# Performance work log

Hardware: AMD Instinct MI355X
Metric: run time of the kernel (lower is better)

Reference implementation:

```python
import jax, jax.numpy as jnp
import numpy as np

N, DIM, T = 4096, 100, 50
DT = np.float32(1.0 / T)          # delta_t = total_time / num_time_interval
R = 1.0                           # fbsde._R
Q = 1.0                           # state cost in h_th
DELTA_CLIP = 50.0
UMIN, UMAX = -1.0, 1.0            # config.u_threhold_min/max
EPS = 1e-6                        # BatchNorm eps


def _bn(x, w, b):
    # BatchNorm1d in training mode: batch stats, biased variance
    m = jnp.mean(x, axis=0)
    v = jnp.mean((x - m) ** 2, axis=0)
    return (x - m) * jax.lax.rsqrt(v + EPS) * w + b


def _subnet(x, p):
    # FCSubNet: bn -> [linear(no bias) -> bn -> relu] x2 -> linear(bias) -> bn -> /dim
    (bn0_w, bn0_b, w1, bn1_w, bn1_b, w2, bn2_w, bn2_b, w3, b3, bn3_w, bn3_b) = p
    h = _bn(x, bn0_w, bn0_b)
    h = jax.nn.relu(_bn(h @ w1.T, bn1_w, bn1_b))
    h = jax.nn.relu(_bn(h @ w2.T, bn2_w, bn2_b))
    h = h @ w3.T + b3
    return _bn(h, bn3_w, bn3_b) / DIM


def setup_inputs() -> dict:
    key = jax.random.key(0)
    ks = jax.random.split(key, 15)
    s = 0.05  # keep weights small for numerical stability over 50 recurrent steps
    return dict(
        dw=jax.random.normal(ks[0], (N, DIM, T), jnp.float32) * jnp.sqrt(DT),
        y_init=jax.random.uniform(ks[1], (1,), jnp.float32, 0.0, 1.0),
        z_init=jax.random.uniform(ks[2], (1, DIM), jnp.float32, -0.1, 0.1),
        bn0_w=jax.random.uniform(ks[3], (100,), jnp.float32, 0.1, 0.5),
        bn0_b=jax.random.normal(ks[4], (100,), jnp.float32) * 0.1,
        w1=jax.random.normal(ks[5], (110, 100), jnp.float32) * s,
        bn1_w=jax.random.uniform(ks[6], (110,), jnp.float32, 0.1, 0.5),
        bn1_b=jax.random.normal(ks[7], (110,), jnp.float32) * 0.1,
        w2=jax.random.normal(ks[8], (110, 110), jnp.float32) * s,
        bn2_w=jax.random.uniform(ks[9], (110,), jnp.float32, 0.1, 0.5),
        bn2_b=jax.random.normal(ks[10], (110,), jnp.float32) * 0.1,
        w3=jax.random.normal(ks[11], (100, 110), jnp.float32) * s,
        b3=jax.random.normal(ks[12], (100,), jnp.float32) * s,
        bn3_w=jax.random.uniform(ks[13], (100,), jnp.float32, 0.1, 0.5),
        bn3_b=jax.random.normal(ks[14], (100,), jnp.float32) * 0.1,
    )


def reference(dw, y_init, z_init, bn0_w, bn0_b, w1, bn1_w, bn1_b, w2, bn2_w, bn2_b,
              w3, b3, bn3_w, bn3_b):
    p = (bn0_w, bn0_b, w1, bn1_w, bn1_b, w2, bn2_w, bn2_b, w3, b3, bn3_w, bn3_b)
    n = dw.shape[0]
    gamma = jnp.ones((n, DIM, 1), dw.dtype)          # fbsde.gamma; sigma@gamma = gamma (sigma=I), G = ones
    y = jnp.broadcast_to(y_init, (n, 1))[:, :, None]  # [n,1,1]
    z = jnp.broadcast_to(z_init, (n, DIM))[:, :, None]  # [n,dim,1]
    x = jnp.zeros((n, DIM, 1), dw.dtype)
    dw_t = jnp.moveaxis(dw, 2, 0)[..., None]          # [T, n, dim, 1]

    def y_update(x, y, z, u, dwi):
        h = 0.5 * (Q * jnp.sum(x * x, axis=1, keepdims=True) + R * u * u)  # h_th -> [n,1,1]
        i2 = DT * jnp.sum(z * gamma, axis=1, keepdims=True) * u
        i3 = jnp.sum(z * dwi, axis=1, keepdims=True)
        return y - DT * h + i2 + i3

    def step(carry, dwi):
        x, y, z = carry
        u = jnp.clip(-(1.0 / R) * jnp.sum(gamma * z, axis=1, keepdims=True), UMIN, UMAX)
        y = y_update(x, y, z, u, dwi)
        # x_{t+1} = x + f(x)*dt + sigma@gamma*u*dt + G*dw ; f(x) = -x
        x_new = x - x * DT + gamma * u * DT + dwi
        z_new = (_subnet(x_new[:, :, 0], p) / DIM)[:, :, None]
        return (x_new, y, z_new), (x[:, :, 0], u[:, 0, 0])

    (x, y, z), (xs, us) = jax.lax.scan(step, (x, y, z), dw_t[:-1])
    # final step t = T-1: only u and y are updated (loop breaks before x/z update)
    u = jnp.clip(-(1.0 / R) * jnp.sum(gamma * z, axis=1, keepdims=True), UMIN, UMAX)
    y = y_update(x, y, z, u, dw_t[-1])
    xs = jnp.concatenate([xs, x[None, :, :, 0]], axis=0)   # [T, n, dim] = totalx
    us = jnp.concatenate([us, u[None, :, 0, 0]], axis=0)   # [T, n]     = totalu

    ye = 0.5 * jnp.sum(x[:, :, 0] ** 2, axis=1, keepdims=True)  # g_th -> [n,1]
    d = y[:, :, 0] - ye
    ad = jnp.abs(d)
    sl1 = jnp.mean(jnp.where(ad < 1.0, 0.5 * d * d, ad - 0.5))  # SmoothL1Loss, beta=1
    loss = 2.0 * DELTA_CLIP * (sl1 + jnp.mean(ye[:, 0]) ** 2)
    return loss, y, ye, xs, us
```

## Files before the change

kernel.cpp:

```cpp
#include <hip/hip_runtime.h>

#define NS    4096
#define DDIM  100
#define HD    110
#define HP    112
#define TSTEPS 50
#define DTc   0.02f
#define EPSc  1e-6f

__global__ void kw_prep(const float* __restrict__ w1, const float* __restrict__ w2,
                        const float* __restrict__ w3,
                        float* __restrict__ wtt1, float* __restrict__ wtt2,
                        float* __restrict__ wtt3) {
  int tid = threadIdx.x;
  for (int idx = tid; idx < 14 * 100 * 8; idx += 256) {
    int jt = idx / 800, r = idx % 800, k = r / 8, jj = r % 8, j = jt * 8 + jj;
    wtt1[idx] = (j < HD) ? w1[j * DDIM + k] : 0.f;
  }
  for (int idx = tid; idx < 14 * 110 * 8; idx += 256) {
    int jt = idx / 880, r = idx % 880, k = r / 8, jj = r % 8, j = jt * 8 + jj;
    wtt2[idx] = (j < HD) ? w2[j * HD + k] : 0.f;
  }
  for (int idx = tid; idx < 13 * 110 * 8; idx += 256) {
    int jt = idx / 880, r = idx % 880, k = r / 8, jj = r % 8, j = jt * 8 + jj;
    wtt3[idx] = (j < DDIM) ? w3[j * HD + k] : 0.f;
  }
}

__global__ __launch_bounds__(256) void kt_dw(const float* __restrict__ dw,
                                             float* __restrict__ dwT) {
  int n = blockIdx.x * 256 + threadIdx.x;
  int d = blockIdx.y;
  const float2* src = (const float2*)(dw + (size_t)n * DDIM * TSTEPS + d * TSTEPS);
  float v[TSTEPS];
#pragma unroll
  for (int i = 0; i < TSTEPS / 2; ++i) {
    float2 p = src[i];
    v[2 * i] = p.x; v[2 * i + 1] = p.y;
  }
#pragma unroll
  for (int t = 0; t < TSTEPS; ++t)
    dwT[((size_t)t * DDIM + d) * NS + n] = v[t];
}

__global__ __launch_bounds__(1024) void ka2(
    int t, int flags,
    const float* __restrict__ dw, const float* __restrict__ dwT,
    const float* __restrict__ y_init, const float* __restrict__ z_init,
    const float* __restrict__ bn3w, const float* __restrict__ bn3b,
    float* __restrict__ x, float* __restrict__ y, const float* __restrict__ h3,
    const float* __restrict__ stats3, float* __restrict__ stats0,
    float* __restrict__ st_zero, float* __restrict__ lacc,
    float* __restrict__ out_y, float* __restrict__ out_ye,
    float* __restrict__ out_xs, float* __restrict__ out_us)
{
  const bool first  = flags & 1;
  const bool last_  = flags & 2;
  const bool usedwt = flags & 4;
  int tid = threadIdx.x, lane = tid & 63, w = tid >> 6;
  int n = blockIdx.x * 64 + lane;
  int d0 = w * 7;
  int nd = DDIM - d0; nd = nd < 0 ? 0 : (nd > 7 ? 7 : nd);

  __shared__ float2 zp[DDIM];
  __shared__ float ps[3][16][64];
  __shared__ float ush[64];
  __shared__ float pst[2][112];

  if (blockIdx.x == 0 && tid < 224) st_zero[tid] = 0.f;
  if (!first && tid < DDIM) {
    float m = stats3[tid] * (1.f / NS);
    float v = stats3[HP + tid] * (1.f / NS) - m * m;
    float istd = rsqrtf(v + EPSc);
    float A = istd * bn3w[tid] * 1e-4f;
    float B = (bn3b[tid] - m * istd * bn3w[tid]) * 1e-4f;
    zp[tid] = make_float2(A, B);
  }
  __syncthreads();

  float xv[7], dwv[7];
  float pz = 0.f, pzdw = 0.f, px2 = 0.f;
#pragma unroll
  for (int i = 0; i < 7; ++i) {
    if (i < nd) {
      int d = d0 + i;
      float zd = first ? z_init[d] : fmaf(h3[d * NS + n], zp[d].x, zp[d].y);
      dwv[i] = usedwt ? dwT[((size_t)t * DDIM + d) * NS + n]
                      : dw[(size_t)n * DDIM * TSTEPS + d * TSTEPS + t];
      xv[i] = first ? 0.f : x[d * NS + n];
      pz += zd;
      pzdw = fmaf(zd, dwv[i], pzdw);
      px2 = fmaf(xv[i], xv[i], px2);
    }
  }
  ps[0][w][lane] = pz; ps[1][w][lane] = pzdw; ps[2][w][lane] = px2;
  __syncthreads();

  if (w == 0) {
    float sz = 0.f, szdw = 0.f, sx2 = 0.f;
#pragma unroll
    for (int k = 0; k < 16; ++k) {
      sz += ps[0][k][lane]; szdw += ps[1][k][lane]; sx2 += ps[2][k][lane];
    }
    float u = fminf(fmaxf(-sz, -1.f), 1.f);
    float yv = first ? y_init[0] : y[n];
    yv += -DTc * 0.5f * (sx2 + u * u) + DTc * sz * u + szdw;
    out_us[t * NS + n] = u;
    ush[lane] = u;
    if (!last_) {
      y[n] = yv;
    } else {
      out_y[n] = yv;
      float ye = 0.5f * sx2;
      out_ye[n] = ye;
      float dd = yv - ye, ad = fabsf(dd);
      float s = ad < 1.f ? 0.5f * dd * dd : ad - 0.5f;
      float q = ye;
      for (int off = 32; off; off >>= 1) {
        s += __shfl_down(s, off);
        q += __shfl_down(q, off);
      }
      if (lane == 0) { atomicAdd(&lacc[0], s); atomicAdd(&lacc[1], q); }
    }
  }
  __syncthreads();

  if (!last_) {
    float u = ush[lane];
#pragma unroll
    for (int i = 0; i < 7; ++i) {
      if (i < nd) {
        int d = d0 + i;
        float xn = fmaf(xv[i], 1.f - DTc, fmaf(u, DTc, dwv[i]));
        x[d * NS + n] = xn;
        out_xs[((size_t)t * NS + n) * DDIM + d] = xv[i];
        float s = xn, q = xn * xn;
        for (int off = 32; off; off >>= 1) {
          s += __shfl_down(s, off);
          q += __shfl_down(q, off);
        }
        if (lane == 0) { pst[0][d] = s; pst[1][d] = q; }
      }
    }
    __syncthreads();
    if (tid < DDIM) atomicAdd(&stats0[tid], pst[0][tid]);
    else if (tid >= 128 && tid < 128 + DDIM) atomicAdd(&stats0[HP + tid - 128], pst[1][tid - 128]);
  } else {
#pragma unroll
    for (int i = 0; i < 7; ++i)
      if (i < nd)
        out_xs[((size_t)t * NS + n) * DDIM + i + d0] = xv[i];
  }
}

template <int KD, int RELU, int HASB>
__global__ __launch_bounds__(64) void km2(
    const float* __restrict__ in, float* __restrict__ out,
    const float* __restrict__ stats_in, float* __restrict__ stats_out,
    float* __restrict__ zero_ptr,
    const float* __restrict__ bnw, const float* __restrict__ bnb,
    const float* __restrict__ wtt, const float* __restrict__ bias, int Jreal)
{
  int tid = threadIdx.x;
  int jt = blockIdx.y;
  int n = blockIdx.x * 64 + tid;

  __shared__ float4 wl[KD * 2];
  __shared__ float2 ab[KD];

  const float4* src = (const float4*)(wtt + (size_t)jt * KD * 8);
  for (int i = tid; i < KD * 2; i += 64) wl[i] = src[i];
  for (int k = tid; k < KD; k += 64) {
    float m = stats_in[k] * (1.f / NS);
    float v = stats_in[HP + k] * (1.f / NS) - m * m;
    float istd = rsqrtf(v + EPSc);
    float A = istd * bnw[k];
    ab[k] = make_float2(A, bnb[k] - m * A);
  }
  if (blockIdx.x == 0 && jt == 0)
    for (int i = tid; i < 224; i += 64) zero_ptr[i] = 0.f;
  __syncthreads();

  float acc[8] = {0, 0, 0, 0, 0, 0, 0, 0};
  const float* ip = in + n;
#pragma unroll 10
  for (int k = 0; k < KD; ++k) {
    float a = ip[(size_t)k * NS];
    float2 p = ab[k];
    a = fmaf(a, p.x, p.y);
    if (RELU) a = fmaxf(a, 0.f);
    float4 wA = wl[2 * k], wB = wl[2 * k + 1];
    acc[0] = fmaf(a, wA.x, acc[0]); acc[1] = fmaf(a, wA.y, acc[1]);
    acc[2] = fmaf(a, wA.z, acc[2]); acc[3] = fmaf(a, wA.w, acc[3]);
    acc[4] = fmaf(a, wB.x, acc[4]); acc[5] = fmaf(a, wB.y, acc[5]);
    acc[6] = fmaf(a, wB.z, acc[6]); acc[7] = fmaf(a, wB.w, acc[7]);
  }

  int j0 = jt * 8;
#pragma unroll
  for (int jj = 0; jj < 8; ++jj) {
    int j = j0 + jj;
    if (j < Jreal) {
      float vv = acc[jj] + (HASB ? bias[j] : 0.f);
      out[j * NS + n] = vv;
      float s = vv, q = vv * vv;
      for (int off = 32; off; off >>= 1) {
        s += __shfl_down(s, off);
        q += __shfl_down(q, off);
      }
      if (tid == 0) {
        atomicAdd(&stats_out[j], s);
        atomicAdd(&stats_out[HP + j], q);
      }
    }
  }
}

__global__ void k_loss(const float* __restrict__ lacc, float* __restrict__ out_loss) {
  float sl1 = lacc[0] * (1.f / NS);
  float mye = lacc[1] * (1.f / NS);
  out_loss[0] = 100.f * (sl1 + mye * mye);
}

extern "C" void kernel_launch(void* const* d_in, const int* in_sizes, int n_in,
                              void* d_out, int out_size, void* d_ws, size_t ws_size,
                              hipStream_t stream) {
  const float* dw     = (const float*)d_in[0];
  const float* y_init = (const float*)d_in[1];
  const float* z_init = (const float*)d_in[2];
  const float* bn0w   = (const float*)d_in[3];
  const float* bn0b   = (const float*)d_in[4];
  const float* w1     = (const float*)d_in[5];
  const float* bn1w   = (const float*)d_in[6];
  const float* bn1b   = (const float*)d_in[7];
  const float* w2     = (const float*)d_in[8];
  const float* bn2w   = (const float*)d_in[9];
  const float* bn2b   = (const float*)d_in[10];
  const float* w3     = (const float*)d_in[11];
  const float* b3     = (const float*)d_in[12];
  const float* bn3w   = (const float*)d_in[13];
  const float* bn3b   = (const float*)d_in[14];

  float* ws  = (float*)d_ws;
  float* x   = ws;
  float* y   = x + 409600;
  float* h1  = y + 4096;
  float* h2  = h1 + (size_t)HP * NS;
  float* h3  = h2 + (size_t)HP * NS;
  float* st  = h3 + (size_t)HP * NS;
  float* st0 = st, *st1 = st + 224, *st2 = st + 448, *st3 = st + 672;
  float* lacc = st + 896;
  float* wtt1 = lacc + 8;
  float* wtt2 = wtt1 + 14 * 100 * 8;
  float* wtt3 = wtt2 + 14 * 110 * 8;
  float* dwT  = wtt3 + 13 * 110 * 8;
  size_t need_dwt = ((size_t)(dwT - ws) + (size_t)TSTEPS * DDIM * NS) * sizeof(float);
  bool usedwt = ws_size >= need_dwt;

  float* out      = (float*)d_out;
  float* out_loss = out;
  float* out_y    = out + 1;
  float* out_ye   = out_y + NS;
  float* out_xs   = out_ye + NS;
  float* out_us   = out_xs + (size_t)TSTEPS * NS * DDIM;

  hipMemsetAsync(st, 0, (896 + 8) * sizeof(float), stream);
  kw_prep<<<1, 256, 0, stream>>>(w1, w2, w3, wtt1, wtt2, wtt3);
  if (usedwt) kt_dw<<<dim3(16, 100), 256, 0, stream>>>(dw, dwT);

  for (int t = 0; t < TSTEPS; ++t) {
    int flags = (t == 0 ? 1 : 0) | (t == TSTEPS - 1 ? 2 : 0) | (usedwt ? 4 : 0);
    ka2<<<64, 1024, 0, stream>>>(t, flags, dw, dwT, y_init, z_init,
                                 bn3w, bn3b, x, y, h3, st3, st0, st2, lacc,
                                 out_y, out_ye, out_xs, out_us);
    if (t < TSTEPS - 1) {
      km2<100, 0, 0><<<dim3(64, 14), 64, 0, stream>>>(
          x, h1, st0, st1, st3, bn0w, bn0b, wtt1, (const float*)nullptr, HD);
      km2<110, 1, 0><<<dim3(64, 14), 64, 0, stream>>>(
          h1, h2, st1, st2, st0, bn1w, bn1b, wtt2, (const float*)nullptr, HD);
      km2<110, 1, 1><<<dim3(64, 13), 64, 0, stream>>>(
          h2, h3, st2, st3, st1, bn2w, bn2b, wtt3, b3, DDIM);
    }
  }
  k_loss<<<1, 1, 0, stream>>>(lacc, out_loss);
}
```

Before: 5.628 ms.

## Fuse all timesteps into one cooperative persistent kernel with grid barriers

```diff
diff --git a/kernel.cpp b/kernel.cpp
--- a/kernel.cpp
+++ b/kernel.cpp
@@ -1,113 +1,125 @@
 #include <hip/hip_runtime.h>
 
-#define NS    4096
-#define DDIM  100
-#define HD    110
-#define HP    112
+#define NS     4096
+#define DDIM   100
+#define HD     110
+#define JP     128
+#define HP     112
 #define TSTEPS 50
-#define DTc   0.02f
-#define EPSc  1e-6f
-
-__global__ void kw_prep(const float* __restrict__ w1, const float* __restrict__ w2,
-                        const float* __restrict__ w3,
-                        float* __restrict__ wtt1, float* __restrict__ wtt2,
-                        float* __restrict__ wtt3) {
-  int tid = threadIdx.x;
-  for (int idx = tid; idx < 14 * 100 * 8; idx += 256) {
-    int jt = idx / 800, r = idx % 800, k = r / 8, jj = r % 8, j = jt * 8 + jj;
-    wtt1[idx] = (j < HD) ? w1[j * DDIM + k] : 0.f;
-  }
-  for (int idx = tid; idx < 14 * 110 * 8; idx += 256) {
-    int jt = idx / 880, r = idx % 880, k = r / 8, jj = r % 8, j = jt * 8 + jj;
-    wtt2[idx] = (j < HD) ? w2[j * HD + k] : 0.f;
-  }
-  for (int idx = tid; idx < 13 * 110 * 8; idx += 256) {
-    int jt = idx / 880, r = idx % 880, k = r / 8, jj = r % 8, j = jt * 8 + jj;
-    wtt3[idx] = (j < DDIM) ? w3[j * HD + k] : 0.f;
-  }
-}
-
-__global__ __launch_bounds__(256) void kt_dw(const float* __restrict__ dw,
-                                             float* __restrict__ dwT) {
-  int n = blockIdx.x * 256 + threadIdx.x;
-  int d = blockIdx.y;
-  const float2* src = (const float2*)(dw + (size_t)n * DDIM * TSTEPS + d * TSTEPS);
-  float v[TSTEPS];
-#pragma unroll
-  for (int i = 0; i < TSTEPS / 2; ++i) {
-    float2 p = src[i];
-    v[2 * i] = p.x; v[2 * i + 1] = p.y;
-  }
-#pragma unroll
-  for (int t = 0; t < TSTEPS; ++t)
-    dwT[((size_t)t * DDIM + d) * NS + n] = v[t];
-}
-
-__global__ __launch_bounds__(1024) void ka2(
-    int t, int flags,
-    const float* __restrict__ dw, const float* __restrict__ dwT,
-    const float* __restrict__ y_init, const float* __restrict__ z_init,
-    const float* __restrict__ bn3w, const float* __restrict__ bn3b,
-    float* __restrict__ x, float* __restrict__ y, const float* __restrict__ h3,
-    const float* __restrict__ stats3, float* __restrict__ stats0,
-    float* __restrict__ st_zero, float* __restrict__ lacc,
-    float* __restrict__ out_y, float* __restrict__ out_ye,
-    float* __restrict__ out_xs, float* __restrict__ out_us)
-{
-  const bool first  = flags & 1;
-  const bool last_  = flags & 2;
-  const bool usedwt = flags & 4;
+#define DTc    0.02f
+#define EPSc   1e-6f
+#define NB     256
+#define BT     512
+
+struct MegaArgs {
+  const float *dw, *y_init, *z_init;
+  const float *bn0w, *bn0b, *w1, *bn1w, *bn1b, *w2, *bn2w, *bn2b, *w3, *b3, *bn3w, *bn3b;
+  float *x, *y, *h1, *h2, *h3;
+  float *st0, *st1, *st2, *st3, *lacc;
+  float *wt1, *wt2, *wt3, *dwT;
+  int *cnt; int usedwt;
+  float *out_loss, *out_y, *out_ye, *out_xs, *out_us;
+};
+
+__device__ __forceinline__ void gbar(int* cnt, int idx) {
+  __syncthreads();
+  if (threadIdx.x == 0) {
+    __threadfence();
+    atomicAdd(&cnt[idx], 1);
+    while (__hip_atomic_load(&cnt[idx], __ATOMIC_RELAXED, __HIP_MEMORY_SCOPE_AGENT) < NB)
+      __builtin_amdgcn_s_sleep(1);
+    __threadfence();
+  }
+  __syncthreads();
+}
+
+__device__ void init_phase(const float* __restrict__ w1, const float* __restrict__ w2,
+                           const float* __restrict__ w3,
+                           float* __restrict__ wt1, float* __restrict__ wt2,
+                           float* __restrict__ wt3,
+                           const float* __restrict__ dw, float* __restrict__ dwT,
+                           int usedwt) {
+  int g = blockIdx.x * BT + threadIdx.x;
+  for (int idx = g; idx < DDIM * JP; idx += NB * BT) {
+    int k = idx >> 7, j = idx & 127;
+    wt1[idx] = (j < HD) ? w1[j * DDIM + k] : 0.f;
+  }
+  for (int idx = g; idx < HD * JP; idx += NB * BT) {
+    int k = idx >> 7, j = idx & 127;
+    wt2[idx] = (j < HD) ? w2[j * HD + k] : 0.f;
+    wt3[idx] = (j < DDIM) ? w3[j * HD + k] : 0.f;
+  }
+  if (usedwt) {
+    int n = g & (NS - 1);
+    int d0 = g >> 12;
+    for (int d = d0; d < DDIM; d += 32) {
+      const float2* src = (const float2*)(dw + (size_t)n * DDIM * TSTEPS + d * TSTEPS);
+      float v[TSTEPS];
+#pragma unroll
+      for (int i = 0; i < TSTEPS / 2; ++i) { float2 p = src[i]; v[2*i] = p.x; v[2*i+1] = p.y; }
+#pragma unroll
+      for (int tt = 0; tt < TSTEPS; ++tt)
+        dwT[((size_t)tt * DDIM + d) * NS + n] = v[tt];
+    }
+  }
+}
+
+template <int LAST>
+__device__ void p0_phase(int t, int first, int usedwt,
+                         const float* __restrict__ dwT, const float* __restrict__ dwraw,
+                         const float* __restrict__ y_init, const float* __restrict__ z_init,
+                         const float* __restrict__ bn3w, const float* __restrict__ bn3b,
+                         float* __restrict__ x, float* __restrict__ y,
+                         const float* __restrict__ h3, const float* __restrict__ st3,
+                         float* __restrict__ st0, float* __restrict__ lacc,
+                         float* __restrict__ out_y, float* __restrict__ out_ye,
+                         float* __restrict__ out_xs, float* __restrict__ out_us,
+                         float2* zp, float* ps, float* ush, float* zero_target) {
   int tid = threadIdx.x, lane = tid & 63, w = tid >> 6;
-  int n = blockIdx.x * 64 + lane;
-  int d0 = w * 7;
-  int nd = DDIM - d0; nd = nd < 0 ? 0 : (nd > 7 ? 7 : nd);
-
-  __shared__ float2 zp[DDIM];
-  __shared__ float ps[3][16][64];
-  __shared__ float ush[64];
-  __shared__ float pst[2][112];
-
-  if (blockIdx.x == 0 && tid < 224) st_zero[tid] = 0.f;
+  int bid = blockIdx.x;
+  if (bid >= 64) {
+    if (bid == 64 && tid < 2 * HP) zero_target[tid] = 0.f;
+    return;
+  }
+  int n = bid * 64 + lane;
   if (!first && tid < DDIM) {
-    float m = stats3[tid] * (1.f / NS);
-    float v = stats3[HP + tid] * (1.f / NS) - m * m;
+    float m = st3[tid] * (1.f / NS);
+    float v = st3[HP + tid] * (1.f / NS) - m * m;
     float istd = rsqrtf(v + EPSc);
     float A = istd * bn3w[tid] * 1e-4f;
     float B = (bn3b[tid] - m * istd * bn3w[tid]) * 1e-4f;
     zp[tid] = make_float2(A, B);
   }
   __syncthreads();
-
-  float xv[7], dwv[7];
+  int d0 = w * 13;
+  int cd = DDIM - d0; cd = cd > 13 ? 13 : cd;
+  float xr[13], dwr[13];
   float pz = 0.f, pzdw = 0.f, px2 = 0.f;
 #pragma unroll
-  for (int i = 0; i < 7; ++i) {
-    if (i < nd) {
-      int d = d0 + i;
-      float zd = first ? z_init[d] : fmaf(h3[d * NS + n], zp[d].x, zp[d].y);
-      dwv[i] = usedwt ? dwT[((size_t)t * DDIM + d) * NS + n]
-                      : dw[(size_t)n * DDIM * TSTEPS + d * TSTEPS + t];
-      xv[i] = first ? 0.f : x[d * NS + n];
-      pz += zd;
-      pzdw = fmaf(zd, dwv[i], pzdw);
-      px2 = fmaf(xv[i], xv[i], px2);
-    }
-  }
-  ps[0][w][lane] = pz; ps[1][w][lane] = pzdw; ps[2][w][lane] = px2;
-  __syncthreads();
-
+  for (int i = 0; i < 13; ++i) if (i < cd) {
+    int d = d0 + i;
+    float zd = first ? z_init[d] : fmaf(h3[(size_t)d * NS + n], zp[d].x, zp[d].y);
+    dwr[i] = usedwt ? dwT[((size_t)t * DDIM + d) * NS + n]
+                    : dwraw[(size_t)n * DDIM * TSTEPS + d * TSTEPS + t];
+    xr[i] = first ? 0.f : x[(size_t)d * NS + n];
+    pz += zd; pzdw = fmaf(zd, dwr[i], pzdw); px2 = fmaf(xr[i], xr[i], px2);
+  }
+  ps[(0 * 8 + w) * 64 + lane] = pz;
+  ps[(1 * 8 + w) * 64 + lane] = pzdw;
+  ps[(2 * 8 + w) * 64 + lane] = px2;
+  __syncthreads();
   if (w == 0) {
     float sz = 0.f, szdw = 0.f, sx2 = 0.f;
 #pragma unroll
-    for (int k = 0; k < 16; ++k) {
-      sz += ps[0][k][lane]; szdw += ps[1][k][lane]; sx2 += ps[2][k][lane];
+    for (int k = 0; k < 8; ++k) {
+      sz += ps[k * 64 + lane]; szdw += ps[(8 + k) * 64 + lane]; sx2 += ps[(16 + k) * 64 + lane];
     }
     float u = fminf(fmaxf(-sz, -1.f), 1.f);
     float yv = first ? y_init[0] : y[n];
     yv += -DTc * 0.5f * (sx2 + u * u) + DTc * sz * u + szdw;
     out_us[t * NS + n] = u;
     ush[lane] = u;
-    if (!last_) {
+    if (!LAST) {
       y[n] = yv;
     } else {
       out_y[n] = yv;
@@ -116,171 +128,162 @@
       float dd = yv - ye, ad = fabsf(dd);
       float s = ad < 1.f ? 0.5f * dd * dd : ad - 0.5f;
       float q = ye;
-      for (int off = 32; off; off >>= 1) {
-        s += __shfl_down(s, off);
-        q += __shfl_down(q, off);
+      for (int off = 32; off; off >>= 1) { s += __shfl_down(s, off); q += __shfl_down(q, off); }
+      if (lane == 0) { atomicAdd(&lacc[0], s); atomicAdd(&lacc[1], q); }
+    }
+  }
+  __syncthreads();
+  if (!LAST) {
+    float u = ush[lane];
+#pragma unroll
+    for (int i = 0; i < 13; ++i) if (i < cd) {
+      int d = d0 + i;
+      float xn = fmaf(xr[i], 1.f - DTc, fmaf(u, DTc, dwr[i]));
+      x[(size_t)d * NS + n] = xn;
+      out_xs[((size_t)t * NS + n) * DDIM + d] = xr[i];
+      float s = xn, q = xn * xn;
+      for (int off = 32; off; off >>= 1) { s += __shfl_down(s, off); q += __shfl_down(q, off); }
+      if (lane == 0) { atomicAdd(&st0[d], s); atomicAdd(&st0[HP + d], q); }
+    }
+  } else {
+#pragma unroll
+    for (int i = 0; i < 13; ++i) if (i < cd)
+      out_xs[((size_t)(TSTEPS - 1) * NS + n) * DDIM + d0 + i] = xr[i];
+  }
+}
+
+template <int KD, int RELU, int HASB>
+__device__ void gemm_phase(const float* __restrict__ in, float* __restrict__ out,
+                           const float* __restrict__ stats_in, float* __restrict__ stats_out,
+                           const float* __restrict__ bnw, const float* __restrict__ bnb,
+                           const float* __restrict__ wt, const float* __restrict__ bias,
+                           int Jreal, float* ldsx, float2* ldsab, float* zero_target) {
+  int tid = threadIdx.x, lane = tid & 63, w = tid >> 6;
+  int n0 = (blockIdx.x & 63) * 64;
+  int jq = blockIdx.x >> 6;
+  if (tid < KD) {
+    float m = stats_in[tid] * (1.f / NS);
+    float v = stats_in[HP + tid] * (1.f / NS) - m * m;
+    float A = rsqrtf(v + EPSc) * bnw[tid];
+    ldsab[tid] = make_float2(A, bnb[tid] - m * A);
+  }
+  for (int k = w; k < KD; k += 8)
+    ldsx[k * 64 + lane] = in[(size_t)k * NS + n0 + lane];
+  if (blockIdx.x == 64 && w == 7) {
+    for (int i = lane; i < 2 * HP; i += 64) zero_target[i] = 0.f;
+  }
+  __syncthreads();
+  if (w < 7) {
+    int j0 = __builtin_amdgcn_readfirstlane(jq * 28 + w * 4);
+    const float* wp = wt + j0;
+    float a0 = 0.f, a1 = 0.f, a2 = 0.f, a3 = 0.f;
+#pragma unroll 5
+    for (int k = 0; k < KD; ++k) {
+      float a = ldsx[k * 64 + lane];
+      float2 p = ldsab[k];
+      a = fmaf(a, p.x, p.y);
+      if (RELU) a = fmaxf(a, 0.f);
+      const float* wr = wp + k * JP;
+      a0 = fmaf(a, wr[0], a0); a1 = fmaf(a, wr[1], a1);
+      a2 = fmaf(a, wr[2], a2); a3 = fmaf(a, wr[3], a3);
+    }
+    float acc[4] = {a0, a1, a2, a3};
+#pragma unroll
+    for (int i = 0; i < 4; ++i) {
+      int j = j0 + i;
+      if (j < Jreal) {
+        float vv = acc[i] + (HASB ? bias[j] : 0.f);
+        out[(size_t)j * NS + n0 + lane] = vv;
+        float s = vv, q = vv * vv;
+        for (int off = 32; off; off >>= 1) { s += __shfl_down(s, off); q += __shfl_down(q, off); }
+        if (lane == 0) { atomicAdd(&stats_out[j], s); atomicAdd(&stats_out[HP + j], q); }
       }
-      if (lane == 0) { atomicAdd(&lacc[0], s); atomicAdd(&lacc[1], q); }
-    }
-  }
-  __syncthreads();
-
-  if (!last_) {
-    float u = ush[lane];
-#pragma unroll
-    for (int i = 0; i < 7; ++i) {
-      if (i < nd) {
-        int d = d0 + i;
-        float xn = fmaf(xv[i], 1.f - DTc, fmaf(u, DTc, dwv[i]));
-        x[d * NS + n] = xn;
-        out_xs[((size_t)t * NS + n) * DDIM + d] = xv[i];
-        float s = xn, q = xn * xn;
-        for (int off = 32; off; off >>= 1) {
-          s += __shfl_down(s, off);
-          q += __shfl_down(q, off);
-        }
-        if (lane == 0) { pst[0][d] = s; pst[1][d] = q; }
-      }
-    }
-    __syncthreads();
-    if (tid < DDIM) atomicAdd(&stats0[tid], pst[0][tid]);
-    else if (tid >= 128 && tid < 128 + DDIM) atomicAdd(&stats0[HP + tid - 128], pst[1][tid - 128]);
-  } else {
-#pragma unroll
-    for (int i = 0; i < 7; ++i)
-      if (i < nd)
-        out_xs[((size_t)t * NS + n) * DDIM + i + d0] = xv[i];
-  }
-}
-
-template <int KD, int RELU, int HASB>
-__global__ __launch_bounds__(64) void km2(
-    const float* __restrict__ in, float* __restrict__ out,
-    const float* __restrict__ stats_in, float* __restrict__ stats_out,
-    float* __restrict__ zero_ptr,
-    const float* __restrict__ bnw, const float* __restrict__ bnb,
-    const float* __restrict__ wtt, const float* __restrict__ bias, int Jreal)
-{
-  int tid = threadIdx.x;
-  int jt = blockIdx.y;
-  int n = blockIdx.x * 64 + tid;
-
-  __shared__ float4 wl[KD * 2];
-  __shared__ float2 ab[KD];
-
-  const float4* src = (const float4*)(wtt + (size_t)jt * KD * 8);
-  for (int i = tid; i < KD * 2; i += 64) wl[i] = src[i];
-  for (int k = tid; k < KD; k += 64) {
-    float m = stats_in[k] * (1.f / NS);
-    float v = stats_in[HP + k] * (1.f / NS) - m * m;
-    float istd = rsqrtf(v + EPSc);
-    float A = istd * bnw[k];
-    ab[k] = make_float2(A, bnb[k] - m * A);
-  }
-  if (blockIdx.x == 0 && jt == 0)
-    for (int i = tid; i < 224; i += 64) zero_ptr[i] = 0.f;
-  __syncthreads();
-
-  float acc[8] = {0, 0, 0, 0, 0, 0, 0, 0};
-  const float* ip = in + n;
-#pragma unroll 10
-  for (int k = 0; k < KD; ++k) {
-    float a = ip[(size_t)k * NS];
-    float2 p = ab[k];
-    a = fmaf(a, p.x, p.y);
-    if (RELU) a = fmaxf(a, 0.f);
-    float4 wA = wl[2 * k], wB = wl[2 * k + 1];
-    acc[0] = fmaf(a, wA.x, acc[0]); acc[1] = fmaf(a, wA.y, acc[1]);
-    acc[2] = fmaf(a, wA.z, acc[2]); acc[3] = fmaf(a, wA.w, acc[3]);
-    acc[4] = fmaf(a, wB.x, acc[4]); acc[5] = fmaf(a, wB.y, acc[5]);
-    acc[6] = fmaf(a, wB.z, acc[6]); acc[7] = fmaf(a, wB.w, acc[7]);
-  }
-
-  int j0 = jt * 8;
-#pragma unroll
-  for (int jj = 0; jj < 8; ++jj) {
-    int j = j0 + jj;
-    if (j < Jreal) {
-      float vv = acc[jj] + (HASB ? bias[j] : 0.f);
-      out[j * NS + n] = vv;
-      float s = vv, q = vv * vv;
-      for (int off = 32; off; off >>= 1) {
-        s += __shfl_down(s, off);
-        q += __shfl_down(q, off);
-      }
-      if (tid == 0) {
-        atomicAdd(&stats_out[j], s);
-        atomicAdd(&stats_out[HP + j], q);
-      }
-    }
-  }
-}
-
-__global__ void k_loss(const float* __restrict__ lacc, float* __restrict__ out_loss) {
-  float sl1 = lacc[0] * (1.f / NS);
-  float mye = lacc[1] * (1.f / NS);
-  out_loss[0] = 100.f * (sl1 + mye * mye);
+    }
+  }
+}
+
+__global__ __launch_bounds__(BT, 1) void mega(MegaArgs a) {
+  __shared__ float  ldsx[HD * 64];
+  __shared__ float2 ldsab[HP];
+  __shared__ float2 zp[DDIM];
+  __shared__ float  ps[3 * 8 * 64];
+  __shared__ float  ush[64];
+
+  init_phase(a.w1, a.w2, a.w3, a.wt1, a.wt2, a.wt3, a.dw, a.dwT, a.usedwt);
+  int bi = 0;
+  gbar(a.cnt, bi++);
+
+  for (int t = 0; t < TSTEPS - 1; ++t) {
+    p0_phase<0>(t, t == 0, a.usedwt, a.dwT, a.dw, a.y_init, a.z_init, a.bn3w, a.bn3b,
+                a.x, a.y, a.h3, a.st3, a.st0, a.lacc, a.out_y, a.out_ye, a.out_xs, a.out_us,
+                zp, ps, ush, a.st2);
+    gbar(a.cnt, bi++);
+    gemm_phase<DDIM, 0, 0>(a.x,  a.h1, a.st0, a.st1, a.bn0w, a.bn0b, a.wt1, (const float*)0, HD,   ldsx, ldsab, a.st3);
+    gbar(a.cnt, bi++);
+    gemm_phase<HD,   1, 0>(a.h1, a.h2, a.st1, a.st2, a.bn1w, a.bn1b, a.wt2, (const float*)0, HD,   ldsx, ldsab, a.st0);
+    gbar(a.cnt, bi++);
+    gemm_phase<HD,   1, 1>(a.h2, a.h3, a.st2, a.st3, a.bn2w, a.bn2b, a.wt3, a.b3,            DDIM, ldsx, ldsab, a.st1);
+    gbar(a.cnt, bi++);
+  }
+  p0_phase<1>(TSTEPS - 1, 0, a.usedwt, a.dwT, a.dw, a.y_init, a.z_init, a.bn3w, a.bn3b,
+              a.x, a.y, a.h3, a.st3, a.st0, a.lacc, a.out_y, a.out_ye, a.out_xs, a.out_us,
+              zp, ps, ush, a.st2);
+  gbar(a.cnt, bi++);
+  if (blockIdx.x == 0 && threadIdx.x == 0) {
+    float sl1 = a.lacc[0] * (1.f / NS);
+    float mye = a.lacc[1] * (1.f / NS);
+    a.out_loss[0] = 100.f * (sl1 + mye * mye);
+  }
 }
 
 extern "C" void kernel_launch(void* const* d_in, const int* in_sizes, int n_in,
                               void* d_out, int out_size, void* d_ws, size_t ws_size,
                               hipStream_t stream) {
-  const float* dw     = (const float*)d_in[0];
-  const float* y_init = (const float*)d_in[1];
-  const float* z_init = (const float*)d_in[2];
-  const float* bn0w   = (const float*)d_in[3];
-  const float* bn0b   = (const float*)d_in[4];
-  const float* w1     = (const float*)d_in[5];
-  const float* bn1w   = (const float*)d_in[6];
-  const float* bn1b   = (const float*)d_in[7];
-  const float* w2     = (const float*)d_in[8];
-  const float* bn2w   = (const float*)d_in[9];
-  const float* bn2b   = (const float*)d_in[10];
-  const float* w3     = (const float*)d_in[11];
-  const float* b3     = (const float*)d_in[12];
-  const float* bn3w   = (const float*)d_in[13];
-  const float* bn3b   = (const float*)d_in[14];
-
-  float* ws  = (float*)d_ws;
-  float* x   = ws;
-  float* y   = x + 409600;
-  float* h1  = y + 4096;
-  float* h2  = h1 + (size_t)HP * NS;
-  float* h3  = h2 + (size_t)HP * NS;
-  float* st  = h3 + (size_t)HP * NS;
-  float* st0 = st, *st1 = st + 224, *st2 = st + 448, *st3 = st + 672;
-  float* lacc = st + 896;
-  float* wtt1 = lacc + 8;
-  float* wtt2 = wtt1 + 14 * 100 * 8;
-  float* wtt3 = wtt2 + 14 * 110 * 8;
-  float* dwT  = wtt3 + 13 * 110 * 8;
-  size_t need_dwt = ((size_t)(dwT - ws) + (size_t)TSTEPS * DDIM * NS) * sizeof(float);
-  bool usedwt = ws_size >= need_dwt;
-
-  float* out      = (float*)d_out;
-  float* out_loss = out;
-  float* out_y    = out + 1;
-  float* out_ye   = out_y + NS;
-  float* out_xs   = out_ye + NS;
-  float* out_us   = out_xs + (size_t)TSTEPS * NS * DDIM;
-
-  hipMemsetAsync(st, 0, (896 + 8) * sizeof(float), stream);
-  kw_prep<<<1, 256, 0, stream>>>(w1, w2, w3, wtt1, wtt2, wtt3);
-  if (usedwt) kt_dw<<<dim3(16, 100), 256, 0, stream>>>(dw, dwT);
-
-  for (int t = 0; t < TSTEPS; ++t) {
-    int flags = (t == 0 ? 1 : 0) | (t == TSTEPS - 1 ? 2 : 0) | (usedwt ? 4 : 0);
-    ka2<<<64, 1024, 0, stream>>>(t, flags, dw, dwT, y_init, z_init,
-                                 bn3w, bn3b, x, y, h3, st3, st0, st2, lacc,
-                                 out_y, out_ye, out_xs, out_us);
-    if (t < TSTEPS - 1) {
-      km2<100, 0, 0><<<dim3(64, 14), 64, 0, stream>>>(
-          x, h1, st0, st1, st3, bn0w, bn0b, wtt1, (const float*)nullptr, HD);
-      km2<110, 1, 0><<<dim3(64, 14), 64, 0, stream>>>(
-          h1, h2, st1, st2, st0, bn1w, bn1b, wtt2, (const float*)nullptr, HD);
-      km2<110, 1, 1><<<dim3(64, 13), 64, 0, stream>>>(
-          h2, h3, st2, st3, st1, bn2w, bn2b, wtt3, b3, DDIM);
-    }
-  }
-  k_loss<<<1, 1, 0, stream>>>(lacc, out_loss);
-}
+  MegaArgs a;
+  a.dw     = (const float*)d_in[0];
+  a.y_init = (const float*)d_in[1];
+  a.z_init = (const float*)d_in[2];
+  a.bn0w   = (const float*)d_in[3];
+  a.bn0b   = (const float*)d_in[4];
+  a.w1     = (const float*)d_in[5];
+  a.bn1w   = (const float*)d_in[6];
+  a.bn1b   = (const float*)d_in[7];
+  a.w2     = (const float*)d_in[8];
+  a.bn2w   = (const float*)d_in[9];
+  a.bn2b   = (const float*)d_in[10];
+  a.w3     = (const float*)d_in[11];
+  a.b3     = (const float*)d_in[12];
+  a.bn3w   = (const float*)d_in[13];
+  a.bn3b   = (const float*)d_in[14];
+
+  float* ws = (float*)d_ws;
+  size_t off = 0;
+  auto alloc = [&](size_t nf) { float* p = ws + off; off += nf; return p; };
+  a.x    = alloc((size_t)DDIM * NS);
+  a.y    = alloc(NS);
+  a.h1   = alloc((size_t)HP * NS);
+  a.h2   = alloc((size_t)HP * NS);
+  a.h3   = alloc((size_t)HP * NS);
+  a.st0  = alloc(2 * HP);
+  a.st1  = alloc(2 * HP);
+  a.st2  = alloc(2 * HP);
+  a.st3  = alloc(2 * HP);
+  a.lacc = alloc(8);
+  a.cnt  = (int*)alloc(256);
+  a.wt1  = alloc((size_t)DDIM * JP);
+  a.wt2  = alloc((size_t)HD * JP);
+  a.wt3  = alloc((size_t)HD * JP);
+  a.dwT  = alloc((size_t)TSTEPS * DDIM * NS);
+  a.usedwt = (ws_size >= off * sizeof(float)) ? 1 : 0;
+
+  float* out = (float*)d_out;
+  a.out_loss = out;
+  a.out_y    = out + 1;
+  a.out_ye   = a.out_y + NS;
+  a.out_xs   = a.out_ye + NS;
+  a.out_us   = a.out_xs + (size_t)TSTEPS * NS * DDIM;
+
+  hipMemsetAsync(a.st0, 0, (4 * 2 * HP + 8 + 256) * sizeof(float), stream);
+  void* params[] = {&a};
+  hipLaunchCooperativeKernel((const void*)mega, dim3(NB), dim3(BT), params, 0, stream);
+}
```

New measurement: 10.15 ms. 80.4% more time.
